# Optimization experiments

Hardware: AMD Instinct MI355X
Metric: run time of the kernel (lower is better)

## Reference

```python
import jax, jax.numpy as jnp
import numpy as np
import math

B, CIN, H, W = 8, 64, 128, 128
IC = 128           # inter_channel
CMIN = 32
FN = 3             # feature_num
PLANES = CMIN * 2  # BNL planes
GROUPS = 8
ORDER = 2
GAMMA = 1e-4
FEAT_SHAPES = [(64, 128, 128), (128, 64, 64), (256, 32, 32)]

_pm_cache = {}

def _pool_mat(n, s):
    # adaptive avg-pool matrix [s, n] (torch AdaptiveAvgPool2d bin rule)
    key = (n, s)
    if key not in _pm_cache:
        m = np.zeros((s, n), np.float32)
        for j in range(s):
            a = (j * n) // s
            b = -((-(j + 1) * n) // s)
            m[j, a:b] = 1.0 / (b - a)
        _pm_cache[key] = jnp.asarray(m)
    return _pm_cache[key]

def _pap(x):
    # pyramidAP: adaptive avg pool to 1,3,6,8 and flatten -> [b,c,110]
    b, c, hh, ww = x.shape
    outs = []
    for s in (1, 3, 6, 8):
        ph, pw = _pool_mat(hh, s), _pool_mat(ww, s)
        outs.append(jnp.einsum('ph,bchw,qw->bcpq', ph, x, pw).reshape(b, c, s * s))
    return jnp.concatenate(outs, axis=2)

def _c1x1(w, x):
    return jnp.einsum('oi,bihw->bohw', w, x)

def _pad1(x):
    # kernel_size=1, padding=1 conv == 1x1 conv then zero-pad spatially by 1
    return jnp.pad(x, ((0, 0), (0, 0), (1, 1), (1, 1)))

def _conv3(w, x):
    return jax.lax.conv_general_dilated(x, w, (1, 1), 'SAME',
                                        dimension_numbers=('NCHW', 'OIHW', 'NCHW'))

def _bnl(x_high, x_low, t_w, p_w, g_w, z_w, gn_w, gn_b):
    b, c, h, w = x_high.shape
    # per-group flattened 'single token' vectors of length (planes/G)*h*w
    t = _c1x1(t_w, x_high).reshape(b, GROUPS, -1)
    p = _c1x1(p_w, x_low).reshape(b, GROUPS, -1)
    g = _c1x1(g_w, x_low).reshape(b, GROUPS, -1)
    alphas = [math.sqrt((2 * GAMMA) ** k / math.factorial(k) * math.exp(-2 * GAMMA))
              for k in range(ORDER + 1)]
    t_tay = jnp.stack([t ** k * alphas[k] for k in range(ORDER + 1)], axis=2)  # [b,G,3,N]
    p_tay = jnp.stack([p ** k * alphas[k] for k in range(ORDER + 1)], axis=2)
    att = jnp.einsum('bgkn,bgn->bgk', p_tay, g)          # [b,G,3]
    x = jnp.einsum('bgk,bgkn->bgn', att, t_tay).reshape(b, PLANES, h, w)
    # grouped 1x1 conv z (groups=8)
    x = jnp.einsum('goi,bgihw->bgohw', z_w,
                   x.reshape(b, GROUPS, PLANES // GROUPS, h, w)).reshape(b, c, h, w)
    # GroupNorm(8, 64)
    xg = x.reshape(b, GROUPS, -1)
    mu = xg.mean(-1, keepdims=True)
    var = xg.var(-1, keepdims=True)
    xn = ((xg - mu) / jnp.sqrt(var + 1e-5)).reshape(b, c, h, w)
    xn = xn * gn_w[None, :, None, None] + gn_b[None, :, None, None]
    return xn + x_high

def setup_inputs() -> dict:
    key = jax.random.key(0)
    ks = iter(jax.random.split(key, 64))
    def rn(shape, scale=1.0):
        return jax.random.normal(next(ks), shape, jnp.float32) * scale
    inp = {'input_g': rn((B, CIN, H, W)), 'input_c': rn((B, CIN, H, W))}
    for i, (c, hh, ww) in enumerate(FEAT_SHAPES):
        inp[f'fg_{i}'] = rn((B, c, hh, ww))
        inp[f'fc_{i}'] = rn((B, c, hh, ww))
        for nm in ('k1', 'v1', 'k2', 'v2'):
            inp[f'{nm}_w_{i}'] = rn((IC, c), 0.05)
    inp['q1_w'] = rn((IC, CIN, 3, 3), 0.05)
    inp['q2_w'] = rn((IC, CIN, 3, 3), 0.05)
    inp['mask1_w'] = rn((CIN, IC + CIN), 0.05)
    inp['mask2_w'] = rn((CIN, IC + CIN), 0.05)
    inp['fuse1_w'] = rn((CIN, CIN * FN), 0.05)
    inp['fuse2_w'] = rn((CIN, CIN * FN), 0.05)
    inp['t_w'] = rn((PLANES, CIN), 0.05)
    inp['p_w'] = rn((PLANES, CIN), 0.05)
    inp['g_w'] = rn((PLANES, CIN), 0.05)
    inp['z_w'] = rn((GROUPS, CIN // GROUPS, PLANES // GROUPS), 0.05)
    inp['gn_w'] = jnp.ones((CIN,), jnp.float32)
    inp['gn_b'] = jnp.zeros((CIN,), jnp.float32)
    return inp

def reference(input_g, input_c, fg_0, fg_1, fg_2, fc_0, fc_1, fc_2,
              q1_w, q2_w,
              k1_w_0, v1_w_0, k2_w_0, v2_w_0,
              k1_w_1, v1_w_1, k2_w_1, v2_w_1,
              k1_w_2, v1_w_2, k2_w_2, v2_w_2,
              mask1_w, mask2_w, fuse1_w, fuse2_w,
              t_w, p_w, g_w, z_w, gn_w, gn_b):
    b, c, h, w = input_g.shape
    n = h * w
    x_q1 = _conv3(q1_w, input_g).reshape(b, IC, n)
    x_q2 = _conv3(q2_w, input_c).reshape(b, IC, n)
    fgs = [fg_0, fg_1, fg_2]
    fcs = [fc_0, fc_1, fc_2]
    k1s = [k1_w_0, k1_w_1, k1_w_2]
    v1s = [v1_w_0, v1_w_1, v1_w_2]
    k2s = [k2_w_0, k2_w_1, k2_w_2]
    v2s = [v2_w_0, v2_w_1, v2_w_2]
    grays, colors = [], []
    for i in range(FN):
        xk1 = _pap(_pad1(_c1x1(k1s[i], fcs[i])))   # [b,IC,110]
        xk2 = _pap(_pad1(_c1x1(k2s[i], fgs[i])))
        xv1 = _pap(_pad1(_c1x1(v1s[i], fcs[i])))
        xv2 = _pap(_pad1(_c1x1(v2s[i], fgs[i])))
        kq1 = jax.nn.softmax(jnp.clip(jnp.einsum('bcp,bcn->bpn', xk1, x_q1), -64, 64), axis=1)
        kq2 = jax.nn.softmax(jnp.clip(jnp.einsum('bcp,bcn->bpn', xk2, x_q2), -64, 64), axis=1)
        vkq1 = jnp.einsum('bcp,bpn->bcn', xv1, kq1).reshape(b, IC, h, w)
        vkq2 = jnp.einsum('bcp,bpn->bcn', xv2, kq2).reshape(b, IC, h, w)
        grays.append(_c1x1(mask1_w, jnp.concatenate([input_g, vkq1], 1)))
        colors.append(_c1x1(mask2_w, jnp.concatenate([input_c, vkq2], 1)))
    x_gray = jnp.tanh(_c1x1(fuse1_w, jnp.concatenate(grays, 1))) + input_g
    x_color = jnp.tanh(_c1x1(fuse2_w, jnp.concatenate(colors, 1))) + input_c
    return _bnl(x_gray, x_color, t_w, p_w, g_w, z_w, gn_w, gn_b) + input_g
```

## Files before the change

kernel.cpp:

```cpp
#include <hip/hip_runtime.h>
#include <math.h>

constexpr int    BB      = 8;
constexpr int    NN      = 16384;
constexpr size_t SZ_XQ_ST = (size_t)BB * 128 * NN;
constexpr size_t SZ_XF_ST = (size_t)BB * 64 * NN;

constexpr size_t OFF_XQ   = 0;
constexpr size_t OFF_XT   = 16777216;
constexpr size_t OFF_XF   = 33554432;
constexpr size_t OFF_XG   = OFF_XF + 8388608;
constexpr size_t OFF_POOL = OFF_XF + 2 * SZ_XF_ST;
constexpr size_t OFF_XK   = OFF_POOL + 788480;
constexpr size_t OFF_XV   = OFF_XK + 344064;
constexpr size_t OFF_MT   = OFF_XV + 688128;
constexpr size_t OFF_W    = OFF_MT + 393216;
constexpr size_t OFF_AT   = OFF_W + 73728;
constexpr size_t OFF_WT   = OFF_AT + 4096;
constexpr size_t OFF_ATTC = OFF_WT + 12288;
constexpr size_t OFF_MV   = OFF_ATTC + 192;
constexpr size_t OFF_PART = OFF_MV + 128;
constexpr size_t OFF_PART2= OFF_PART + 98304;

#define A0SQ 0.9998000199986667f
#define A1SQ 1.9996000399973335e-4f
#define A2SQ 1.9996000399973334e-8f

typedef __attribute__((ext_vector_type(8))) short bf16x8;
typedef __attribute__((ext_vector_type(4))) float f32x4;

__device__ inline ushort f2bf(float f) {
    uint u = __float_as_uint(f);
    return (ushort)((u + 0x7fffu + ((u >> 16) & 1u)) >> 16);
}
__device__ inline float bf2f(ushort u) { return __uint_as_float((uint)u << 16); }
__device__ inline uint pk2bf(float lo, float hi) {
    return (uint)f2bf(lo) | ((uint)f2bf(hi) << 16);
}

__global__ __launch_bounds__(256) void k_xt(const float* __restrict__ in0, const float* __restrict__ in1,
                                            ushort* __restrict__ xt0, ushort* __restrict__ xt1) {
    __shared__ float L[64 * 130];
    const int y = blockIdx.x, b = blockIdx.y, tid = threadIdx.x;
    const float* in = blockIdx.z ? in1 : in0;
    ushort* xt = blockIdx.z ? xt1 : xt0;
    const float* ib = in + (((size_t)b * 64) << 14) + (y << 7);
    for (int r = 0; r < 32; ++r) {
        int idx = tid + (r << 8); int ch = idx >> 7; int x = idx & 127;
        L[ch * 130 + x] = ib[((size_t)ch << 14) + x];
    }
    __syncthreads();
    const int x = tid >> 1, seg = tid & 1;
    ushort* ob = xt + ((size_t)(b * 128 + y) * 128 + x) * 64 + seg * 32;
    uint pk[16];
#pragma unroll
    for (int c = 0; c < 16; ++c)
        pk[c] = pk2bf(L[(seg * 32 + 2 * c) * 130 + x], L[(seg * 32 + 2 * c + 1) * 130 + x]);
    uint4* o4 = (uint4*)ob;
#pragma unroll
    for (int c = 0; c < 4; ++c) o4[c] = make_uint4(pk[4 * c], pk[4 * c + 1], pk[4 * c + 2], pk[4 * c + 3]);
}

__global__ __launch_bounds__(256) void k_wt(const float* __restrict__ w1, const float* __restrict__ w2,
                                            ushort* __restrict__ wt1, ushort* __restrict__ wt2) {
    int id = blockIdx.x * 256 + threadIdx.x;
    if (id >= 147456) return;
    int cs = id / 73728; int rem = id - cs * 73728;
    int t = rem >> 13; int oc = (rem >> 6) & 127; int ic = rem & 63;
    const float* w = cs ? w2 : w1;
    (cs ? wt2 : wt1)[rem] = f2bf(w[((size_t)(oc * 64 + ic)) * 9 + t]);
}

__global__ __launch_bounds__(256, 2) void k_convm2(const ushort* __restrict__ Xt0, const ushort* __restrict__ Xt1,
                                                   const ushort* __restrict__ Wt0, const ushort* __restrict__ Wt1,
                                                   ushort* __restrict__ out_base) {
    __shared__ ushort smem[3 * 130 * 72];
    const int tid = threadIdx.x;
    const int y = blockIdx.x, b = blockIdx.y;
    const ushort* Xt = blockIdx.z ? Xt1 : Xt0;
    const ushort* Wt = blockIdx.z ? Wt1 : Wt0;
    ushort* out = out_base + (size_t)blockIdx.z * 16777216;
    const int l = tid & 63;
    const int wv = __builtin_amdgcn_readfirstlane(tid >> 6);
    const int lr = l & 15;
    const int q = l >> 4;

    for (int slot = tid; slot < 390; slot += 256) {
        int dy = slot / 130, xx = slot - dy * 130;
        int row = y + dy - 1, sx = xx - 1;
        bool v = (row >= 0) & (row < 128) & (sx >= 0) & (sx < 128);
        const uint4* s = (const uint4*)(Xt + (((size_t)(b * 128 + row) * 128 + sx) * 64));
        uint4* d = (uint4*)(smem + (size_t)slot * 72);
        uint4 z = make_uint4(0, 0, 0, 0);
#pragma unroll
        for (int j = 0; j < 8; ++j) d[j] = v ? s[j] : z;
    }
    __syncthreads();

    f32x4 acc[2][8];
#pragma unroll
    for (int f = 0; f < 2; ++f)
#pragma unroll
        for (int g = 0; g < 8; ++g)
#pragma unroll
            for (int r = 0; r < 4; ++r) acc[f][g][r] = 0.f;

#pragma unroll
    for (int t = 0; t < 9; ++t) {
        const int dy = t / 3, dx = t - dy * 3;
#pragma unroll
        for (int h = 0; h < 2; ++h) {
            const int ko = h * 32 + q * 8;
            bf16x8 a0 = *(const bf16x8*)(Wt + ((size_t)(t * 128 + wv * 32 + lr) * 64 + ko));
            bf16x8 a1 = *(const bf16x8*)(Wt + ((size_t)(t * 128 + wv * 32 + 16 + lr) * 64 + ko));
#pragma unroll
            for (int g = 0; g < 8; ++g) {
                bf16x8 bb = *(const bf16x8*)(smem + (size_t)(dy * 130 + g * 16 + lr + dx) * 72 + ko);
                acc[0][g] = __builtin_amdgcn_mfma_f32_16x16x32_bf16(a0, bb, acc[0][g], 0, 0, 0);
                acc[1][g] = __builtin_amdgcn_mfma_f32_16x16x32_bf16(a1, bb, acc[1][g], 0, 0, 0);
            }
        }
    }
    __syncthreads();
    uint* T = (uint*)smem;
#pragma unroll
    for (int f = 0; f < 2; ++f)
#pragma unroll
        for (int g = 0; g < 8; ++g) {
            int dw = (g * 16 + lr) * 68 + wv * 16 + f * 8 + q * 2;
            T[dw] = pk2bf(acc[f][g][0], acc[f][g][1]);
            T[dw + 1] = pk2bf(acc[f][g][2], acc[f][g][3]);
        }
    __syncthreads();
    const int x = tid >> 1, sg = tid & 1;
    ushort* ob = out + ((size_t)(b * 128 + y) * 128 + x) * 128 + sg * 64;
    const uint* src = &T[x * 68 + sg * 32];
#pragma unroll
    for (int j = 0; j < 8; ++j) {
        uint4 vv = *(const uint4*)(src + 4 * j);
        *(uint4*)(ob + j * 8) = vv;
    }
}

struct PoolPtrs { const float* src[6]; };

__global__ __launch_bounds__(256) void k_pool(PoolPtrs pp, float* __restrict__ ws) {
    extern __shared__ float P[];
    const int plane = blockIdx.x;
    const int tid = threadIdx.x;
    int tI, h; size_t toff; int base;
    if      (plane < 512)  { tI = 0; h = 128; toff = 0;      base = 0;    }
    else if (plane < 1536) { tI = 1; h = 64;  toff = 56320;  base = 512;  }
    else if (plane < 3584) { tI = 2; h = 32;  toff = 168960; base = 1536; }
    else if (plane < 4096) { tI = 3; h = 128; toff = 394240; base = 3584; }
    else if (plane < 5120) { tI = 4; h = 64;  toff = 450560; base = 4096; }
    else                   { tI = 5; h = 32;  toff = 563200; base = 5120; }
    const int local = plane - base;
    const float* img = pp.src[tI] + (size_t)local * h * h;
    const int stride = h + 1;
    const int hh = h * h;
    for (int f = tid; f < hh; f += 256) {
        int r = f / h; int cc = f - r * h;
        P[r * stride + cc] = img[f];
    }
    __syncthreads();
    if (tid < h) {
        float cur = 0.f; const int rb = tid * stride;
        for (int cc = 0; cc < h; ++cc) { cur += P[rb + cc]; P[rb + cc] = cur; }
    }
    __syncthreads();
    if (tid < h) {
        float cur = 0.f;
        for (int r = 0; r < h; ++r) { int a = r * stride + tid; cur += P[a]; P[a] = cur; }
    }
    __syncthreads();
    if (tid < 110) {
        int s, off2;
        if (tid == 0)      { s = 1; off2 = 0; }
        else if (tid < 10) { s = 3; off2 = 1; }
        else if (tid < 46) { s = 6; off2 = 10; }
        else               { s = 8; off2 = 46; }
        int r = tid - off2; int j = r / s; int q = r - j * s;
        const int n = h + 2;
        int ra = (j * n) / s,       rb2 = ((j + 1) * n + s - 1) / s;
        int ca = (q * n) / s,       cb2 = ((q + 1) * n + s - 1) / s;
        float area = (float)((rb2 - ra) * (cb2 - ca));
        int r0 = ra - 1; if (r0 < 0) r0 = 0;  int r1 = rb2 - 1; if (r1 > h) r1 = h;
        int c0 = ca - 1; if (c0 < 0) c0 = 0;  int c1 = cb2 - 1; if (c1 > h) c1 = h;
        float ssum = 0.f;
        if (r1 > r0 && c1 > c0) {
            int ri = r1 - 1, rj = r0 - 1, ci = c1 - 1, cj = c0 - 1;
            float f11 = P[ri * stride + ci];
            float f01 = (rj < 0) ? 0.f : P[rj * stride + ci];
            float f10 = (cj < 0) ? 0.f : P[ri * stride + cj];
            float f00 = (rj < 0 || cj < 0) ? 0.f : P[rj * stride + cj];
            ssum = f11 - f01 - f10 + f00;
        }
        ws[OFF_POOL + toff + (size_t)local * 110 + tid] = ssum / area;
    }
}

__global__ __launch_bounds__(256) void k_pkw(const float* __restrict__ f1, const float* __restrict__ f2,
                                             const float* __restrict__ m1, const float* __restrict__ m2,
                                             const float* __restrict__ tw, const float* __restrict__ pw,
                                             const float* __restrict__ gw, float* __restrict__ ws) {
    int id = blockIdx.x * 256 + threadIdx.x;
    if (id < 73728) {
        int c = id % 192; int t = id / 192; int o = t & 63; int t2 = t >> 6; int i = t2 % 3; int st = t2 / 3;
        const float* fu = st ? f2 : f1; const float* ma = st ? m2 : m1;
        float s = 0.f;
        for (int k = 0; k < 64; ++k) s = fmaf(fu[o * 192 + i * 64 + k], ma[k * 192 + c], s);
        ws[OFF_W + id] = s;
    } else if (id < 81920) {
        int x = id - 73728; int o = x & 63; int c = (x >> 6) & 63; int st = x >> 12;
        const float* fu = st ? f2 : f1; const float* ma = st ? m2 : m1;
        float s = 0.f;
        for (int k = 0; k < 192; ++k) s = fmaf(fu[o * 192 + k], ma[(k & 63) * 192 + c], s);
        ((ushort*)(ws + OFF_AT))[(size_t)st * 4096 + o * 64 + c] = f2bf(s);
    } else if (id < 94208) {
        int x = id - 81920; int c = x & 63; int o = (x >> 6) & 63; int f = x >> 12;
        const float* src = (f == 0) ? tw : ((f == 1) ? pw : gw);
        ((ushort*)(ws + OFF_WT))[(size_t)f * 4096 + o * 64 + c] = f2bf(src[o * 64 + c]);
    }
}

struct KvPtrs { const float* k1[3]; const float* k2[3]; const float* v1[3]; const float* v2[3]; };

__global__ __launch_bounds__(256) void k_xkxv(KvPtrs kp, float* __restrict__ ws) {
    int id = blockIdx.x * 256 + threadIdx.x;
    int isV = 0;
    if (id >= 688128) { isV = 1; id -= 688128; }
    int p = id % 112; int t1 = id / 112; int C = t1 & 127; int t2 = t1 >> 7;
    int b = t2 & 7; int t3 = t2 >> 3; int i = t3 % 3; int st = t3 / 3;
    const int ci = 64 << i;
    size_t poff = (size_t)st * 394240 + (i >= 1 ? 56320 : 0) + (i >= 2 ? 112640 : 0);
    const float* kw = isV ? (st ? kp.v2[i] : kp.v1[i]) : (st ? kp.k2[i] : kp.k1[i]);
    float s = 0.f;
    if (p < 110) {
        const float* pl = ws + OFF_POOL + poff + (size_t)b * ci * 110 + p;
        for (int ic = 0; ic < ci; ++ic) s = fmaf(kw[C * ci + ic], pl[(size_t)ic * 110], s);
    }
    if (isV) ws[OFF_XV + id] = s;
    else     ((ushort*)(ws + OFF_XK))[(size_t)t2 * 14336 + p * 128 + C] = f2bf(s);
}

__global__ __launch_bounds__(256) void k_mt(float* __restrict__ ws) {
    int id = blockIdx.x * 256 + threadIdx.x;
    int p = id & 127; int o = (id >> 7) & 63; int t2 = id >> 13;
    int sti = t2 >> 3;
    float s = 0.f;
    if (p < 110) {
        const float* Wrow = ws + OFF_W + ((size_t)sti * 64 + o) * 192 + 64;
        const float* xv = ws + OFF_XV + (size_t)t2 * 128 * 112 + p;
        for (int r = 0; r < 128; ++r) s = fmaf(Wrow[r], xv[(size_t)r * 112], s);
    }
    ((ushort*)(ws + OFF_MT))[id] = f2bf(s);
}

__global__ __launch_bounds__(256, 2) void k_attn5(float* __restrict__ ws,
                                                  const float* __restrict__ g_in,
                                                  const float* __restrict__ c_in) {
    __shared__ uint pbuf[128 * 68];
    const int tid = threadIdx.x;
    const int w = __builtin_amdgcn_readfirstlane(tid >> 6);
    const int l = tid & 63;
    const int lr = l & 15;
    const int g4 = l >> 4;
    const int n0 = blockIdx.x << 7;
    const int b = blockIdx.y;
    const int st = blockIdx.z;

    const ushort* xqb = (const ushort*)(ws + OFF_XQ);
    const ushort* xkb = (const ushort*)(ws + OFF_XK);
    const ushort* mtb = (const ushort*)(ws + OFF_MT);
    const ushort* atb = (const ushort*)(ws + OFF_AT) + (size_t)st * 4096;
    const ushort* xt  = (const ushort*)(ws + OFF_XT) + (size_t)st * 8388608 + ((size_t)b << 14) * 64;
    ushort* xfb       = (ushort*)(ws + OFF_XF) + (size_t)st * 8388608 + ((size_t)b << 14) * 64;

    {
        int row = w * 32 + (l >> 1);
        int dcol = 56 + ((l & 1) << 2);
#pragma unroll
        for (int j = 0; j < 4; ++j) pbuf[row * 68 + dcol + j] = 0;
    }
    const int ng0 = n0 + (2 * w + 0) * 16 + lr;
    const int ng1 = n0 + (2 * w + 1) * 16 + lr;
    const int row0 = w * 32 + lr;
    const int row1 = w * 32 + 16 + lr;

    bf16x8 bq[2][4];
    {
        const ushort* p0 = xqb + ((size_t)(st * 8 + b) * 16384 + ng0) * 128 + g4 * 8;
        const ushort* p1 = xqb + ((size_t)(st * 8 + b) * 16384 + ng1) * 128 + g4 * 8;
#pragma unroll
        for (int kk = 0; kk < 4; ++kk) { bq[0][kk] = *(const bf16x8*)(p0 + kk * 32); bq[1][kk] = *(const bf16x8*)(p1 + kk * 32); }
    }

    f32x4 pacc[4][2];
#pragma unroll
    for (int m = 0; m < 4; ++m)
#pragma unroll
        for (int nt = 0; nt < 2; ++nt)
#pragma unroll
            for (int r = 0; r < 4; ++r) pacc[m][nt][r] = 0.f;

#pragma unroll
    for (int kk = 0; kk < 2; ++kk) {
        bf16x8 bi0 = *(const bf16x8*)(xt + (size_t)ng0 * 64 + kk * 32 + g4 * 8);
        bf16x8 bi1 = *(const bf16x8*)(xt + (size_t)ng1 * 64 + kk * 32 + g4 * 8);
#pragma unroll
        for (int m = 0; m < 4; ++m) {
            bf16x8 a = *(const bf16x8*)(atb + (m * 16 + lr) * 64 + kk * 32 + g4 * 8);
            pacc[m][0] = __builtin_amdgcn_mfma_f32_16x16x32_bf16(a, bi0, pacc[m][0], 0, 0, 0);
            pacc[m][1] = __builtin_amdgcn_mfma_f32_16x16x32_bf16(a, bi1, pacc[m][1], 0, 0, 0);
        }
    }

#pragma unroll 1
    for (int i = 0; i < 3; ++i) {
        const ushort* xk = xkb + (size_t)((st * 3 + i) * 8 + b) * 14336 + (size_t)lr * 128 + g4 * 8;
        const ushort* mt_p = mtb + (size_t)((st * 3 + i) * 8 + b) * 8192 + (size_t)lr * 128 + g4 * 8;
        f32x4 sacc[7][2];
#pragma unroll
        for (int m = 0; m < 7; ++m)
#pragma unroll
            for (int nt = 0; nt < 2; ++nt)
#pragma unroll
                for (int r = 0; r < 4; ++r) sacc[m][nt][r] = 0.f;
        bf16x8 ac[7], an[7];
#pragma unroll
        for (int m = 0; m < 7; ++m) ac[m] = *(const bf16x8*)(xk + (size_t)(m * 16) * 128);
        __builtin_amdgcn_s_setprio(1);
#pragma unroll
        for (int kk = 0; kk < 4; ++kk) {
            if (kk < 3) {
#pragma unroll
                for (int m = 0; m < 7; ++m) an[m] = *(const bf16x8*)(xk + (size_t)(m * 16) * 128 + (kk + 1) * 32);
            }
#pragma unroll
            for (int m = 0; m < 7; ++m) {
                sacc[m][0] = __builtin_amdgcn_mfma_f32_16x16x32_bf16(ac[m], bq[0][kk], sacc[m][0], 0, 0, 0);
                sacc[m][1] = __builtin_amdgcn_mfma_f32_16x16x32_bf16(ac[m], bq[1][kk], sacc[m][1], 0, 0, 0);
            }
            if (kk < 3) {
#pragma unroll
                for (int m = 0; m < 7; ++m) ac[m] = an[m];
            }
        }
        __builtin_amdgcn_s_setprio(0);
        bf16x8 mc[4], mn[4];
#pragma unroll
        for (int m = 0; m < 4; ++m) mc[m] = *(const bf16x8*)(mt_p + (size_t)(m * 16) * 128);
#pragma unroll
        for (int nt = 0; nt < 2; ++nt) {
            float mx = -3.0e38f;
#pragma unroll
            for (int m = 0; m < 7; ++m)
#pragma unroll
                for (int r = 0; r < 4; ++r) {
                    int p = m * 16 + g4 * 4 + r;
                    float s = fminf(fmaxf(sacc[m][nt][r], -64.f), 64.f);
                    if (p >= 110) s = -3.0e38f;
                    sacc[m][nt][r] = s;
                    mx = fmaxf(mx, s);
                }
            mx = fmaxf(mx, __shfl_xor(mx, 16));
            mx = fmaxf(mx, __shfl_xor(mx, 32));
            float sum = 0.f;
#pragma unroll
            for (int m = 0; m < 7; ++m)
#pragma unroll
                for (int r = 0; r < 4; ++r) {
                    float e = __expf(sacc[m][nt][r] - mx);
                    sacc[m][nt][r] = e;
                    sum += e;
                }
            sum += __shfl_xor(sum, 16);
            sum += __shfl_xor(sum, 32);
            float inv = 1.f / sum;
            const int rowNT = (nt == 0) ? row0 : row1;
#pragma unroll
            for (int m = 0; m < 7; ++m) {
                int dw = rowNT * 68 + m * 8 + g4 * 2;
                pbuf[dw] = pk2bf(sacc[m][nt][0] * inv, sacc[m][nt][1] * inv);
                pbuf[dw + 1] = pk2bf(sacc[m][nt][2] * inv, sacc[m][nt][3] * inv);
            }
        }
        __builtin_amdgcn_s_setprio(1);
#pragma unroll
        for (int kk = 0; kk < 4; ++kk) {
            if (kk < 3) {
#pragma unroll
                for (int m = 0; m < 4; ++m) mn[m] = *(const bf16x8*)(mt_p + (size_t)(m * 16) * 128 + (kk + 1) * 32);
            }
            bf16x8 pb0 = *(const bf16x8*)((const ushort*)pbuf + (size_t)row0 * 136 + kk * 32 + g4 * 8);
            bf16x8 pb1 = *(const bf16x8*)((const ushort*)pbuf + (size_t)row1 * 136 + kk * 32 + g4 * 8);
#pragma unroll
            for (int m = 0; m < 4; ++m) {
                pacc[m][0] = __builtin_amdgcn_mfma_f32_16x16x32_bf16(mc[m], pb0, pacc[m][0], 0, 0, 0);
                pacc[m][1] = __builtin_amdgcn_mfma_f32_16x16x32_bf16(mc[m], pb1, pacc[m][1], 0, 0, 0);
            }
            if (kk < 3) {
#pragma unroll
                for (int m = 0; m < 4; ++m) mc[m] = mn[m];
            }
        }
        __builtin_amdgcn_s_setprio(0);
    }
    const float* ginf = (st ? c_in : g_in) + (((size_t)b * 64) << 14);
    ushort* thb = (ushort*)(ws + OFF_XG) + ((size_t)b << 14) * 64;
#pragma unroll
    for (int nt = 0; nt < 2; ++nt) {
        const int ng = (nt == 0) ? ng0 : ng1;
#pragma unroll
        for (int m = 0; m < 4; ++m) {
            float th[4], o4[4];
#pragma unroll
            for (int r = 0; r < 4; ++r) {
                int o = m * 16 + g4 * 4 + r;
                float v = pacc[m][nt][r];
                float xx = fminf(fmaxf(v, -15.f), 15.f);
                float e = __expf(2.f * xx);
                th[r] = __fdividef(e - 1.f, e + 1.f);
                o4[r] = th[r] + ginf[((size_t)o << 14) + ng];
            }
            *(uint2*)(xfb + (size_t)ng * 64 + m * 16 + g4 * 4) =
                make_uint2(pk2bf(o4[0], o4[1]), pk2bf(o4[2], o4[3]));
            if (st == 0)
                *(uint2*)(thb + (size_t)ng * 64 + m * 16 + g4 * 4) =
                    make_uint2(pk2bf(th[0], th[1]), pk2bf(th[2], th[3]));
        }
    }
}

__global__ __launch_bounds__(256) void k_tpg(float* __restrict__ ws) {
    const int tid = threadIdx.x;
    const int w = __builtin_amdgcn_readfirstlane(tid >> 6);
    const int l = tid & 63;
    const int lr = l & 15;
    const int g4 = l >> 4;
    const int nb = blockIdx.x; const int n0 = nb << 7; const int b = blockIdx.y;

    const ushort* xfg = (const ushort*)(ws + OFF_XF) + ((size_t)b << 14) * 64;
    const ushort* xfc = xfg + 8388608;
    const ushort* wtb = (const ushort*)(ws + OFF_WT);
    float* tf = ws + OFF_XQ + ((size_t)b << 14) * 64;

    float s[4][3];
#pragma unroll
    for (int m = 0; m < 4; ++m) { s[m][0] = 0.f; s[m][1] = 0.f; s[m][2] = 0.f; }

#pragma unroll 1
    for (int nt = 0; nt < 2; ++nt) {
        const int ng = n0 + (2 * w + nt) * 16 + lr;
        f32x4 at_[4], ap_[4], ag_[4];
#pragma unroll
        for (int m = 0; m < 4; ++m)
#pragma unroll
            for (int r = 0; r < 4; ++r) { at_[m][r] = 0.f; ap_[m][r] = 0.f; ag_[m][r] = 0.f; }
#pragma unroll
        for (int kk = 0; kk < 2; ++kk) {
            bf16x8 bg = *(const bf16x8*)(xfg + (size_t)ng * 64 + kk * 32 + g4 * 8);
            bf16x8 bc = *(const bf16x8*)(xfc + (size_t)ng * 64 + kk * 32 + g4 * 8);
#pragma unroll
            for (int m = 0; m < 4; ++m) {
                const int ao = (m * 16 + lr) * 64 + kk * 32 + g4 * 8;
                bf16x8 a_t = *(const bf16x8*)(wtb + ao);
                bf16x8 a_p = *(const bf16x8*)(wtb + 4096 + ao);
                bf16x8 a_g = *(const bf16x8*)(wtb + 8192 + ao);
                at_[m] = __builtin_amdgcn_mfma_f32_16x16x32_bf16(a_t, bg, at_[m], 0, 0, 0);
                ap_[m] = __builtin_amdgcn_mfma_f32_16x16x32_bf16(a_p, bc, ap_[m], 0, 0, 0);
                ag_[m] = __builtin_amdgcn_mfma_f32_16x16x32_bf16(a_g, bc, ag_[m], 0, 0, 0);
            }
        }
#pragma unroll
        for (int m = 0; m < 4; ++m)
#pragma unroll
            for (int r = 0; r < 4; ++r) {
                int o = m * 16 + g4 * 4 + r;
                tf[((size_t)o << 14) + ng] = at_[m][r];
                float pv = ap_[m][r], gv = ag_[m][r];
                s[m][0] += gv;
                s[m][1] = fmaf(pv, gv, s[m][1]);
                s[m][2] = fmaf(pv * pv, gv, s[m][2]);
            }
    }
#pragma unroll
    for (int off = 1; off < 32; off <<= 1)
#pragma unroll
        for (int m = 0; m < 4; ++m)
#pragma unroll
            for (int k = 0; k < 3; ++k) s[m][k] += __shfl_xor(s[m][k], off);
    if (l == 0 || l == 32) {
        const int h = g4 >> 1;
#pragma unroll
        for (int m = 0; m < 4; ++m)
#pragma unroll
            for (int k = 0; k < 3; ++k)
                ws[OFF_PART + (size_t)((b * 8 + 2 * m + h) * 3 + k) * 512 + nb * 4 + w] = s[m][k];
    }
}

__global__ __launch_bounds__(64) void k_attc(float* __restrict__ ws) {
    const int id = blockIdx.x;
    const int l = threadIdx.x;
    const float4* v = (const float4*)(ws + OFF_PART + (size_t)id * 512 + l * 8);
    float4 a = v[0], b2 = v[1];
    float s = a.x + a.y + a.z + a.w + b2.x + b2.y + b2.z + b2.w;
#pragma unroll
    for (int off = 1; off < 64; off <<= 1) s += __shfl_xor(s, off);
    if (l == 0) ws[OFF_ATTC + id] = s;
}

__global__ __launch_bounds__(256) void k_stats2(float* __restrict__ ws, const float* __restrict__ zw) {
    __shared__ float r0[256], r1[256];
    const int nc = blockIdx.x, g = blockIdx.y, b = blockIdx.z, tid = threadIdx.x;
    const float* tf = ws + OFF_XQ + ((size_t)(b * 64 + g * 8) << 14);
    const float* a = ws + OFF_ATTC + (size_t)(b * 8 + g) * 3;
    const float c0 = A0SQ * a[0], c1 = A1SQ * a[1], c2 = A2SQ * a[2];
    const float* z = zw + (size_t)g * 64;
    float sum = 0.f, ssq = 0.f;
    for (int n = nc * 2048 + tid; n < (nc + 1) * 2048; n += 256) {
        float y[8];
#pragma unroll
        for (int pl = 0; pl < 8; ++pl) { float tv = tf[((size_t)pl << 14) + n]; y[pl] = fmaf(fmaf(c2, tv, c1), tv, c0); }
#pragma unroll
        for (int o = 0; o < 8; ++o) {
            float xz = 0.f;
#pragma unroll
            for (int i2 = 0; i2 < 8; ++i2) xz = fmaf(z[o * 8 + i2], y[i2], xz);
            sum += xz; ssq = fmaf(xz, xz, ssq);
        }
    }
    r0[tid] = sum; r1[tid] = ssq;
    __syncthreads();
    for (int w = 128; w > 0; w >>= 1) {
        if (tid < w) { r0[tid] += r0[tid + w]; r1[tid] += r1[tid + w]; }
        __syncthreads();
    }
    if (tid == 0) {
        float* p2 = ws + OFF_PART2 + (size_t)((b * 8 + g) * 8 + nc) * 2;
        p2[0] = r0[0]; p2[1] = r1[0];
    }
}

__global__ __launch_bounds__(64) void k_mv(float* __restrict__ ws) {
    const int t = threadIdx.x;
    float sum = 0.f, ssq = 0.f;
    const float* p2 = ws + OFF_PART2 + (size_t)t * 16;
#pragma unroll
    for (int nc = 0; nc < 8; ++nc) { sum += p2[nc * 2]; ssq += p2[nc * 2 + 1]; }
    float mean = sum * (1.f / 131072.f);
    float var = ssq * (1.f / 131072.f) - mean * mean;
    float* mv = ws + OFF_MV + (size_t)t * 2;
    mv[0] = mean; mv[1] = rsqrtf(var + 1e-5f);
}

__global__ __launch_bounds__(256) void k_final(float* __restrict__ ws, const float* __restrict__ zw,
                                               const float* __restrict__ gnw, const float* __restrict__ gnb,
                                               const float* __restrict__ g_in, float* __restrict__ out) {
    int id = blockIdx.x * 256 + threadIdx.x;
    int n = id & 16383; int g = (id >> 14) & 7; int b = id >> 17;
    const float* a = ws + OFF_ATTC + (size_t)(b * 8 + g) * 3;
    const float c0 = A0SQ * a[0], c1 = A1SQ * a[1], c2 = A2SQ * a[2];
    const float* mv = ws + OFF_MV + (size_t)(b * 8 + g) * 2;
    const float mean = mv[0], istd = mv[1];
    const float* z = zw + (size_t)g * 64;
    const float* tf = ws + OFF_XQ + ((size_t)(b * 64 + g * 8) << 14) + n;
    float y[8];
#pragma unroll
    for (int pl = 0; pl < 8; ++pl) { float tv = tf[(size_t)pl << 14]; y[pl] = fmaf(fmaf(c2, tv, c1), tv, c0); }
    const ushort* thb = (const ushort*)(ws + OFF_XG) + (((size_t)b << 14) + n) * 64 + g * 8;
    ushort4 u0 = *(const ushort4*)thb;
    ushort4 u1 = *(const ushort4*)(thb + 4);
    float thv[8] = { bf2f(u0.x), bf2f(u0.y), bf2f(u0.z), bf2f(u0.w),
                     bf2f(u1.x), bf2f(u1.y), bf2f(u1.z), bf2f(u1.w) };
    const size_t cb = ((size_t)(b * 64 + g * 8) << 14) + n;
    const float* gi = g_in + cb;
    float* op = out + cb;
#pragma unroll
    for (int o = 0; o < 8; ++o) {
        float xz = 0.f;
#pragma unroll
        for (int i2 = 0; i2 < 8; ++i2) xz = fmaf(z[o * 8 + i2], y[i2], xz);
        int ch = g * 8 + o;
        float base = fmaf((xz - mean) * istd, gnw[ch], gnb[ch]) + thv[o];
        op[(size_t)o << 14] = fmaf(2.f, gi[(size_t)o << 14], base);
    }
}

extern "C" void kernel_launch(void* const* d_in, const int* in_sizes, int n_in,
                              void* d_out, int out_size, void* d_ws, size_t ws_size,
                              hipStream_t stream) {
    const float* in_g = (const float*)d_in[0];
    const float* in_c = (const float*)d_in[1];
    float* ws = (float*)d_ws;
    float* out = (float*)d_out;

    ushort* xqb  = (ushort*)(ws + OFF_XQ);
    ushort* xt_g = (ushort*)(ws + OFF_XT);
    ushort* xt_c = xt_g + 8388608;
    ushort* wt_g = (ushort*)(ws + OFF_XF);
    ushort* wt_c = wt_g + 73728;

    k_xt<<<dim3(128, 8, 2), 256, 0, stream>>>(in_g, in_c, xt_g, xt_c);
    k_wt<<<576, 256, 0, stream>>>((const float*)d_in[20], (const float*)d_in[21], wt_g, wt_c);

    k_convm2<<<dim3(128, 8, 2), 256, 0, stream>>>(xt_g, xt_c, wt_g, wt_c, xqb);

    PoolPtrs pp;
    pp.src[0] = (const float*)d_in[3];  pp.src[1] = (const float*)d_in[9];  pp.src[2] = (const float*)d_in[15];
    pp.src[3] = (const float*)d_in[2];  pp.src[4] = (const float*)d_in[8];  pp.src[5] = (const float*)d_in[14];
    k_pool<<<7168, 256, 128 * 129 * 4, stream>>>(pp, ws);

    k_pkw<<<368, 256, 0, stream>>>((const float*)d_in[24], (const float*)d_in[25],
                                   (const float*)d_in[22], (const float*)d_in[23],
                                   (const float*)d_in[26], (const float*)d_in[27],
                                   (const float*)d_in[28], ws);

    KvPtrs kp;
    kp.k1[0] = (const float*)d_in[4];  kp.k1[1] = (const float*)d_in[10]; kp.k1[2] = (const float*)d_in[16];
    kp.k2[0] = (const float*)d_in[6];  kp.k2[1] = (const float*)d_in[12]; kp.k2[2] = (const float*)d_in[18];
    kp.v1[0] = (const float*)d_in[5];  kp.v1[1] = (const float*)d_in[11]; kp.v1[2] = (const float*)d_in[17];
    kp.v2[0] = (const float*)d_in[7];  kp.v2[1] = (const float*)d_in[13]; kp.v2[2] = (const float*)d_in[19];
    k_xkxv<<<5376, 256, 0, stream>>>(kp, ws);

    k_mt<<<3072, 256, 0, stream>>>(ws);

    k_attn5<<<dim3(128, 8, 2), 256, 0, stream>>>(ws, in_g, in_c);

    k_tpg<<<dim3(128, 8), 256, 0, stream>>>(ws);
    k_attc<<<192, 64, 0, stream>>>(ws);

    k_stats2<<<dim3(8, 8, 8), 256, 0, stream>>>(ws, (const float*)d_in[29]);
    k_mv<<<1, 64, 0, stream>>>(ws);
    k_final<<<4096, 256, 0, stream>>>(ws, (const float*)d_in[29], (const float*)d_in[30],
                                      (const float*)d_in[31], in_g, out);
}
```

Baseline: 577.0 us.

## Fuse t/p/g 1x1 projections into attention epilogue via shared memory

The k_tpg kernel is removed and its work is folded into the attention kernel's epilogue. The fused bf16 outputs (tanh plus residual) now go to LDS instead of a global XF buffer. The same block then runs the t projection (gray path) or the p/g projections and Taylor partial sums (color path) from LDS. This drops a kernel launch and a global write-then-read of two 16M-element bf16 tensors, but adds registers and LDS traffic to a kernel launched with launch_bounds(256,2). The t output buffer moves from the XQ region to the XF region.

```diff
diff --git a/kernel.cpp b/kernel.cpp
--- a/kernel.cpp
+++ b/kernel.cpp
@@ -257,7 +257,7 @@
     ((ushort*)(ws + OFF_MT))[id] = f2bf(s);
 }
 
-__global__ __launch_bounds__(256, 2) void k_attn5(float* __restrict__ ws,
+__global__ __launch_bounds__(256, 2) void k_attn7(float* __restrict__ ws,
                                                   const float* __restrict__ g_in,
                                                   const float* __restrict__ c_in) {
     __shared__ uint pbuf[128 * 68];
@@ -275,7 +275,6 @@
     const ushort* mtb = (const ushort*)(ws + OFF_MT);
     const ushort* atb = (const ushort*)(ws + OFF_AT) + (size_t)st * 4096;
     const ushort* xt  = (const ushort*)(ws + OFF_XT) + (size_t)st * 8388608 + ((size_t)b << 14) * 64;
-    ushort* xfb       = (ushort*)(ws + OFF_XF) + (size_t)st * 8388608 + ((size_t)b << 14) * 64;
 
     {
         int row = w * 32 + (l >> 1);
@@ -412,6 +411,7 @@
 #pragma unroll
     for (int nt = 0; nt < 2; ++nt) {
         const int ng = (nt == 0) ? ng0 : ng1;
+        const int rowNT = (nt == 0) ? row0 : row1;
 #pragma unroll
         for (int m = 0; m < 4; ++m) {
             float th[4], o4[4];
@@ -424,80 +424,91 @@
                 th[r] = __fdividef(e - 1.f, e + 1.f);
                 o4[r] = th[r] + ginf[((size_t)o << 14) + ng];
             }
-            *(uint2*)(xfb + (size_t)ng * 64 + m * 16 + g4 * 4) =
-                make_uint2(pk2bf(o4[0], o4[1]), pk2bf(o4[2], o4[3]));
+            int dw = rowNT * 68 + m * 8 + g4 * 2;
+            pbuf[dw] = pk2bf(o4[0], o4[1]);
+            pbuf[dw + 1] = pk2bf(o4[2], o4[3]);
             if (st == 0)
                 *(uint2*)(thb + (size_t)ng * 64 + m * 16 + g4 * 4) =
                     make_uint2(pk2bf(th[0], th[1]), pk2bf(th[2], th[3]));
         }
     }
-}
-
-__global__ __launch_bounds__(256) void k_tpg(float* __restrict__ ws) {
-    const int tid = threadIdx.x;
-    const int w = __builtin_amdgcn_readfirstlane(tid >> 6);
-    const int l = tid & 63;
-    const int lr = l & 15;
-    const int g4 = l >> 4;
-    const int nb = blockIdx.x; const int n0 = nb << 7; const int b = blockIdx.y;
-
-    const ushort* xfg = (const ushort*)(ws + OFF_XF) + ((size_t)b << 14) * 64;
-    const ushort* xfc = xfg + 8388608;
     const ushort* wtb = (const ushort*)(ws + OFF_WT);
-    float* tf = ws + OFF_XQ + ((size_t)b << 14) * 64;
-
-    float s[4][3];
-#pragma unroll
-    for (int m = 0; m < 4; ++m) { s[m][0] = 0.f; s[m][1] = 0.f; s[m][2] = 0.f; }
-
-#pragma unroll 1
-    for (int nt = 0; nt < 2; ++nt) {
-        const int ng = n0 + (2 * w + nt) * 16 + lr;
-        f32x4 at_[4], ap_[4], ag_[4];
-#pragma unroll
-        for (int m = 0; m < 4; ++m)
-#pragma unroll
-            for (int r = 0; r < 4; ++r) { at_[m][r] = 0.f; ap_[m][r] = 0.f; ag_[m][r] = 0.f; }
-#pragma unroll
-        for (int kk = 0; kk < 2; ++kk) {
-            bf16x8 bg = *(const bf16x8*)(xfg + (size_t)ng * 64 + kk * 32 + g4 * 8);
-            bf16x8 bc = *(const bf16x8*)(xfc + (size_t)ng * 64 + kk * 32 + g4 * 8);
-#pragma unroll
-            for (int m = 0; m < 4; ++m) {
-                const int ao = (m * 16 + lr) * 64 + kk * 32 + g4 * 8;
-                bf16x8 a_t = *(const bf16x8*)(wtb + ao);
-                bf16x8 a_p = *(const bf16x8*)(wtb + 4096 + ao);
-                bf16x8 a_g = *(const bf16x8*)(wtb + 8192 + ao);
-                at_[m] = __builtin_amdgcn_mfma_f32_16x16x32_bf16(a_t, bg, at_[m], 0, 0, 0);
-                ap_[m] = __builtin_amdgcn_mfma_f32_16x16x32_bf16(a_p, bc, ap_[m], 0, 0, 0);
-                ag_[m] = __builtin_amdgcn_mfma_f32_16x16x32_bf16(a_g, bc, ag_[m], 0, 0, 0);
-            }
-        }
-#pragma unroll
-        for (int m = 0; m < 4; ++m)
-#pragma unroll
-            for (int r = 0; r < 4; ++r) {
-                int o = m * 16 + g4 * 4 + r;
-                tf[((size_t)o << 14) + ng] = at_[m][r];
-                float pv = ap_[m][r], gv = ag_[m][r];
-                s[m][0] += gv;
-                s[m][1] = fmaf(pv, gv, s[m][1]);
-                s[m][2] = fmaf(pv * pv, gv, s[m][2]);
-            }
-    }
-#pragma unroll
-    for (int off = 1; off < 32; off <<= 1)
-#pragma unroll
-        for (int m = 0; m < 4; ++m)
-#pragma unroll
-            for (int k = 0; k < 3; ++k) s[m][k] += __shfl_xor(s[m][k], off);
-    if (l == 0 || l == 32) {
-        const int h = g4 >> 1;
-#pragma unroll
-        for (int m = 0; m < 4; ++m)
-#pragma unroll
-            for (int k = 0; k < 3; ++k)
-                ws[OFF_PART + (size_t)((b * 8 + 2 * m + h) * 3 + k) * 512 + nb * 4 + w] = s[m][k];
+    if (st == 0) {
+        float* tf = ws + OFF_XF + ((size_t)b << 14) * 64;
+#pragma unroll
+        for (int nt = 0; nt < 2; ++nt) {
+            const int ng = (nt == 0) ? ng0 : ng1;
+            const int rowNT = (nt == 0) ? row0 : row1;
+            f32x4 at_[4];
+#pragma unroll
+            for (int m = 0; m < 4; ++m)
+#pragma unroll
+                for (int r = 0; r < 4; ++r) at_[m][r] = 0.f;
+#pragma unroll
+            for (int kk = 0; kk < 2; ++kk) {
+                bf16x8 bx = *(const bf16x8*)((const ushort*)pbuf + (size_t)rowNT * 136 + kk * 32 + g4 * 8);
+#pragma unroll
+                for (int m = 0; m < 4; ++m) {
+                    bf16x8 a_t = *(const bf16x8*)(wtb + (m * 16 + lr) * 64 + kk * 32 + g4 * 8);
+                    at_[m] = __builtin_amdgcn_mfma_f32_16x16x32_bf16(a_t, bx, at_[m], 0, 0, 0);
+                }
+            }
+#pragma unroll
+            for (int m = 0; m < 4; ++m)
+#pragma unroll
+                for (int r = 0; r < 4; ++r) {
+                    int o = m * 16 + g4 * 4 + r;
+                    tf[((size_t)o << 14) + ng] = at_[m][r];
+                }
+        }
+    } else {
+        float s[4][3];
+#pragma unroll
+        for (int m = 0; m < 4; ++m) { s[m][0] = 0.f; s[m][1] = 0.f; s[m][2] = 0.f; }
+#pragma unroll
+        for (int nt = 0; nt < 2; ++nt) {
+            const int rowNT = (nt == 0) ? row0 : row1;
+            f32x4 ap_[4], ag_[4];
+#pragma unroll
+            for (int m = 0; m < 4; ++m)
+#pragma unroll
+                for (int r = 0; r < 4; ++r) { ap_[m][r] = 0.f; ag_[m][r] = 0.f; }
+#pragma unroll
+            for (int kk = 0; kk < 2; ++kk) {
+                bf16x8 bx = *(const bf16x8*)((const ushort*)pbuf + (size_t)rowNT * 136 + kk * 32 + g4 * 8);
+#pragma unroll
+                for (int m = 0; m < 4; ++m) {
+                    const int ao = (m * 16 + lr) * 64 + kk * 32 + g4 * 8;
+                    bf16x8 a_p = *(const bf16x8*)(wtb + 4096 + ao);
+                    bf16x8 a_g = *(const bf16x8*)(wtb + 8192 + ao);
+                    ap_[m] = __builtin_amdgcn_mfma_f32_16x16x32_bf16(a_p, bx, ap_[m], 0, 0, 0);
+                    ag_[m] = __builtin_amdgcn_mfma_f32_16x16x32_bf16(a_g, bx, ag_[m], 0, 0, 0);
+                }
+            }
+#pragma unroll
+            for (int m = 0; m < 4; ++m)
+#pragma unroll
+                for (int r = 0; r < 4; ++r) {
+                    float pv = ap_[m][r], gv = ag_[m][r];
+                    s[m][0] += gv;
+                    s[m][1] = fmaf(pv, gv, s[m][1]);
+                    s[m][2] = fmaf(pv * pv, gv, s[m][2]);
+                }
+        }
+#pragma unroll
+        for (int off = 1; off < 32; off <<= 1)
+#pragma unroll
+            for (int m = 0; m < 4; ++m)
+#pragma unroll
+                for (int k = 0; k < 3; ++k) s[m][k] += __shfl_xor(s[m][k], off);
+        if (l == 0 || l == 32) {
+            const int h = g4 >> 1;
+#pragma unroll
+            for (int m = 0; m < 4; ++m)
+#pragma unroll
+                for (int k = 0; k < 3; ++k)
+                    ws[OFF_PART + (size_t)((b * 8 + 2 * m + h) * 3 + k) * 512 + blockIdx.x * 4 + w] = s[m][k];
+        }
     }
 }
 
@@ -515,7 +526,7 @@
 __global__ __launch_bounds__(256) void k_stats2(float* __restrict__ ws, const float* __restrict__ zw) {
     __shared__ float r0[256], r1[256];
     const int nc = blockIdx.x, g = blockIdx.y, b = blockIdx.z, tid = threadIdx.x;
-    const float* tf = ws + OFF_XQ + ((size_t)(b * 64 + g * 8) << 14);
+    const float* tf = ws + OFF_XF + ((size_t)(b * 64 + g * 8) << 14);
     const float* a = ws + OFF_ATTC + (size_t)(b * 8 + g) * 3;
     const float c0 = A0SQ * a[0], c1 = A1SQ * a[1], c2 = A2SQ * a[2];
     const float* z = zw + (size_t)g * 64;
@@ -566,7 +577,7 @@
     const float* mv = ws + OFF_MV + (size_t)(b * 8 + g) * 2;
     const float mean = mv[0], istd = mv[1];
     const float* z = zw + (size_t)g * 64;
-    const float* tf = ws + OFF_XQ + ((size_t)(b * 64 + g * 8) << 14) + n;
+    const float* tf = ws + OFF_XF + ((size_t)(b * 64 + g * 8) << 14) + n;
     float y[8];
 #pragma unroll
     for (int pl = 0; pl < 8; ++pl) { float tv = tf[(size_t)pl << 14]; y[pl] = fmaf(fmaf(c2, tv, c1), tv, c0); }
@@ -627,9 +638,8 @@
 
     k_mt<<<3072, 256, 0, stream>>>(ws);
 
-    k_attn5<<<dim3(128, 8, 2), 256, 0, stream>>>(ws, in_g, in_c);
-
-    k_tpg<<<dim3(128, 8), 256, 0, stream>>>(ws);
+    k_attn7<<<dim3(128, 8, 2), 256, 0, stream>>>(ws, in_g, in_c);
+
     k_attc<<<192, 64, 0, stream>>>(ws);
 
     k_stats2<<<dim3(8, 8, 8), 256, 0, stream>>>(ws, (const float*)d_in[29]);
```

Result: faster. 548.3 us (-5.0%).
